# Optimization experiments

Measured on AMD Instinct MI355X. Metric: run time of the kernel, lower is better.

## Reference

```python
import jax, jax.numpy as jnp
import numpy as np
import math

L_MAX = 2; NRAD = 8; R_CUT = 3.5; N_LAYERS = 4; MUL0 = 32; MUL1 = 16
N_NODES = 20000; N_EDGES = 640000

# Orthonormal (Frobenius) basis of symmetric traceless 3x3 matrices for l=2
# component order: xy, yz, z^2, xz, x^2-y^2
_s2 = 1.0 / math.sqrt(2.0); _s6 = 1.0 / math.sqrt(6.0)
_B = np.zeros((5, 3, 3), dtype=np.float32)
_B[0, 0, 1] = _B[0, 1, 0] = _s2
_B[1, 1, 2] = _B[1, 2, 1] = _s2
_B[2, 0, 0] = _B[2, 1, 1] = -_s6; _B[2, 2, 2] = 2 * _s6
_B[3, 0, 2] = _B[3, 2, 0] = _s2
_B[4, 0, 0] = _s2; _B[4, 1, 1] = -_s2
B2 = jnp.asarray(_B)


def silu(x):
    return x * jax.nn.sigmoid(x)


def cutoff_fn(d):
    # CosineCutoff
    return 0.5 * (jnp.cos(d * math.pi / R_CUT) + 1.0) * (d < R_CUT).astype(d.dtype)


def smearing(d, means, betas):
    # ExpNormalSmearing with CosineCutoff envelope
    dc = jnp.clip(d, 1e-6, R_CUT)[:, None]          # [E,1]
    a = 5.0 / R_CUT
    b = jnp.clip(betas, 1e-6, None)
    return cutoff_fn(dc) * jnp.exp(-b * (jnp.exp(-a * dc) - means) ** 2)  # [E,NRAD]


def sph_harm(rh):
    # real spherical harmonics up to l=2, component normalization, (x,y,z) l=1 order
    y0 = jnp.ones_like(rh[:, :1])
    y1 = math.sqrt(3.0) * rh                                   # [E,3]
    rr = rh[:, :, None] * rh[:, None, :]                       # [E,3,3]
    tr = (rh * rh).sum(-1) / 3.0
    rr = rr - tr[:, None, None] * jnp.eye(3, dtype=rh.dtype)   # traceless
    y2 = math.sqrt(15.0) * jnp.einsum('eij,kij->ek', rr, B2)   # [E,5]
    return jnp.concatenate([y0, y1, y2], axis=-1)              # [E,9]


def _forward(pos, alpha, atom_emb, ne_emb, ne_dw, ne_db, ne_cw, ne_cb,
             means, betas, rad_w1, rad_b1, rad_w2, rad_b2,
             tp_w00, tp_w110, tp_w01, tp_w10, tp_w12,
             self_ws, self_wv, pre_ws, pre_wv, post_ws, post_wv,
             ln_g, ln_b, g_w1, g_b1, g_w2, g_b2, z, edge_index):
    N = pos.shape[0]
    src, dst = edge_index[0], edge_index[1]
    rvec = pos[dst] - pos[src]
    d = jnp.sqrt((rvec * rvec).sum(-1) + 1e-12)                # [E]
    rhat = rvec / d[:, None]

    rbf = smearing(d, means, betas)                            # [E,NRAD]
    # per-l radial coefficients (3 small MLPs, stacked on leading dim)
    h = silu(jnp.einsum('en,lnh->leh', rbf, rad_w1) + rad_b1[:, None, :])
    coeff = jnp.einsum('leh,lho->leo', h, rad_w2) + rad_b2[:, None, :]  # [3,E,1]

    Y = sph_harm(rhat)                                         # [E,9]
    eattr = jnp.concatenate([Y[:, :1] * coeff[0],
                             Y[:, 1:4] * coeff[1],
                             Y[:, 4:9] * coeff[2]], axis=-1)
    eattr = jnp.nan_to_num(eattr, nan=0.0, posinf=0.0, neginf=0.0)

    # AtomEncoder + NeighborEmbedding
    s = atom_emb[z]                                            # [N,32]
    C = cutoff_fn(d)
    W = (rbf @ ne_dw + ne_db) * C[:, None]                     # [E,32]
    xn = ne_emb[z]
    aggr = jax.ops.segment_sum(xn[dst] * W, src, num_segments=N)
    s = jnp.concatenate([s, aggr], axis=-1) @ ne_cw + ne_cb    # [N,32]
    v = jnp.zeros((N, MUL1, 3), dtype=s.dtype)                 # l=1 features

    e0, e1, e2 = eattr[:, :1], eattr[:, 1:4], eattr[:, 4:9]
    Qe = jnp.einsum('ek,kij->eij', e2, B2)                     # l=2 as sym traceless matrix

    for li in range(N_LAYERS):
        ss, vs = s[src], v[src]
        # CG tensor product paths (FullyConnectedTensorProduct node x edge -> node)
        m_s = (ss * e0) @ tp_w00[li] + jnp.einsum('evc,ec->ev', vs, e1) @ tp_w110[li]
        m_v = (jnp.einsum('ei,io->eo', ss, tp_w01[li])[:, :, None] * e1[:, None, :]
               + jnp.einsum('evc,vo->eoc', vs * e0[:, :, None], tp_w10[li])
               + jnp.einsum('evc,vo->eoc', jnp.einsum('eij,evj->evi', Qe, vs), tp_w12[li]))
        # alpha-weighted scatter-add aggregation
        ms = jax.ops.segment_sum(m_s * alpha, dst, num_segments=N)
        mv = jax.ops.segment_sum(m_v * alpha[:, :, None], dst, num_segments=N)
        # self interaction (o3.Linear, block-diag per l)
        s = s @ self_ws[li] + ms
        v = jnp.einsum('nvc,vo->noc', v, self_wv[li]) + mv
        # pre-linear -> gate -> post-linear
        ps = s @ pre_ws[li]                                    # [N,48] scalars+gates
        pv = jnp.einsum('nvc,vo->noc', v, pre_wv[li])
        sc = silu(ps[:, :MUL0])
        g = jax.nn.sigmoid(ps[:, MUL0:])
        v = pv * g[:, :, None]
        s = sc @ post_ws[li]
        v = jnp.einsum('nvc,vo->noc', v, post_wv[li])
        # layernorm on scalar channels
        mu = s.mean(-1, keepdims=True)
        var = ((s - mu) ** 2).mean(-1, keepdims=True)
        s = (s - mu) / jnp.sqrt(var + 1e-5) * ln_g[li] + ln_b[li]
        # geom2s: vector norms -> scalar residual
        vn = jnp.sqrt((v * v).sum(-1) + 1e-12)                 # [N,16]
        delta = silu(vn @ g_w1[li] + g_b1[li]) @ g_w2[li] + g_b2[li]
        s = s + delta
    return jnp.concatenate([s, v.reshape(N, MUL1 * 3)], axis=-1)  # [N,80]


def setup_inputs() -> dict:
    key = jax.random.key(0)
    ks = jax.random.split(key, 40)
    f32 = jnp.float32

    def rn(k, shape, fan):
        return jax.random.normal(k, shape, dtype=f32) / math.sqrt(fan)

    start = math.exp(-R_CUT)
    inp = {
        'pos': jax.random.uniform(ks[0], (N_NODES, 3), dtype=f32) * 10.0,
        'alpha': jax.random.uniform(ks[1], (N_EDGES, 1), dtype=f32),
        'atom_emb': rn(ks[2], (100, MUL0), 1.0),
        'ne_emb': rn(ks[3], (100, MUL0), 1.0),
        'ne_dw': rn(ks[4], (NRAD, MUL0), NRAD), 'ne_db': jnp.zeros((MUL0,), f32),
        'ne_cw': rn(ks[5], (2 * MUL0, MUL0), 2 * MUL0), 'ne_cb': jnp.zeros((MUL0,), f32),
        'means': jnp.linspace(start, 1.0, NRAD, dtype=f32),
        'betas': jnp.full((NRAD,), (2.0 / NRAD * (1.0 - start)) ** (-2), dtype=f32),
        'rad_w1': rn(ks[6], (3, NRAD, 256), NRAD), 'rad_b1': jnp.zeros((3, 256), f32),
        'rad_w2': rn(ks[7], (3, 256, 1), 256), 'rad_b2': jnp.zeros((3, 1), f32),
        'tp_w00': rn(ks[8], (N_LAYERS, MUL0, MUL0), MUL0),
        'tp_w110': rn(ks[9], (N_LAYERS, MUL1, MUL0), MUL1),
        'tp_w01': rn(ks[10], (N_LAYERS, MUL0, MUL1), MUL0),
        'tp_w10': rn(ks[11], (N_LAYERS, MUL1, MUL1), MUL1),
        'tp_w12': rn(ks[12], (N_LAYERS, MUL1, MUL1), MUL1),
        'self_ws': rn(ks[13], (N_LAYERS, MUL0, MUL0), MUL0),
        'self_wv': rn(ks[14], (N_LAYERS, MUL1, MUL1), MUL1),
        'pre_ws': rn(ks[15], (N_LAYERS, MUL0, MUL0 + MUL1), MUL0),
        'pre_wv': rn(ks[16], (N_LAYERS, MUL1, MUL1), MUL1),
        'post_ws': rn(ks[17], (N_LAYERS, MUL0, MUL0), MUL0),
        'post_wv': rn(ks[18], (N_LAYERS, MUL1, MUL1), MUL1),
        'ln_g': jnp.ones((N_LAYERS, MUL0), f32), 'ln_b': jnp.zeros((N_LAYERS, MUL0), f32),
        'g_w1': rn(ks[19], (N_LAYERS, MUL1, MUL1), MUL1), 'g_b1': jnp.zeros((N_LAYERS, MUL1), f32),
        'g_w2': rn(ks[20], (N_LAYERS, MUL1, MUL0), MUL1), 'g_b2': jnp.zeros((N_LAYERS, MUL0), f32),
        'z': jax.random.randint(ks[21], (N_NODES,), 0, 100, dtype=jnp.int32),
        'edge_index': jax.random.randint(ks[22], (2, N_EDGES), 0, N_NODES, dtype=jnp.int32),
    }
    return inp


def reference(pos, alpha, atom_emb, ne_emb, ne_dw, ne_db, ne_cw, ne_cb,
              means, betas, rad_w1, rad_b1, rad_w2, rad_b2,
              tp_w00, tp_w110, tp_w01, tp_w10, tp_w12,
              self_ws, self_wv, pre_ws, pre_wv, post_ws, post_wv,
              ln_g, ln_b, g_w1, g_b1, g_w2, g_b2, z, edge_index):
    return _forward(pos, alpha, atom_emb, ne_emb, ne_dw, ne_db, ne_cw, ne_cb,
                    means, betas, rad_w1, rad_b1, rad_w2, rad_b2,
                    tp_w00, tp_w110, tp_w01, tp_w10, tp_w12,
                    self_ws, self_wv, pre_ws, pre_wv, post_ws, post_wv,
                    ln_g, ln_b, g_w1, g_b1, g_w2, g_b2, z, edge_index)
```

## Files before the change

### kernel.cpp

```cpp
#include <hip/hip_runtime.h>

#define RCUT 3.5f
#define TTAB 2048

static __device__ __forceinline__ float sigmoidf_(float x) { return 1.0f / (1.0f + expf(-x)); }
static __device__ __forceinline__ float siluf(float x) { return x / (1.0f + expf(-x)); }
static __device__ __forceinline__ float san(float x) {
    return ((__float_as_uint(x) & 0x7F800000u) != 0x7F800000u) ? x : 0.f;
}

__global__ __launch_bounds__(256) void k_table(const float* means, const float* betas,
                        const float* rad_w1, const float* rad_b1,
                        const float* rad_w2, const float* rad_b2,
                        const float* ne_dw, const float* ne_db,
                        float* tab) {
    __shared__ float red[3][4];
    int i = blockIdx.x;
    int h = threadIdx.x;
    int lane = h & 63, wv = h >> 6;
    float d  = (float)i * (RCUT / (float)(TTAB - 1));
    float dc = fmaxf(d, 1e-6f);
    float C  = (dc < RCUT) ? 0.5f * (cosf(dc * (3.14159265358979f / RCUT)) + 1.0f) : 0.0f;
    float ex = expf(-(5.0f / RCUT) * dc);
    float rbf[8];
#pragma unroll
    for (int nn = 0; nn < 8; ++nn) {
        float b = fmaxf(betas[nn], 1e-6f);
        float t = ex - means[nn];
        rbf[nn] = C * expf(-b * t * t);
    }
    float con[3];
#pragma unroll
    for (int l = 0; l < 3; ++l) {
        float cc = rad_b1[l * 256 + h];
#pragma unroll
        for (int nn = 0; nn < 8; ++nn) cc += rbf[nn] * rad_w1[(l * 8 + nn) * 256 + h];
        con[l] = siluf(cc) * rad_w2[l * 256 + h];
    }
#pragma unroll
    for (int m = 1; m < 64; m <<= 1) {
        con[0] += __shfl_xor(con[0], m, 64);
        con[1] += __shfl_xor(con[1], m, 64);
        con[2] += __shfl_xor(con[2], m, 64);
    }
    if (lane == 0) { red[0][wv] = con[0]; red[1][wv] = con[1]; red[2][wv] = con[2]; }
    __syncthreads();
    if (h < 3)
        tab[i * 40 + h] = rad_b2[h] + red[h][0] + red[h][1] + red[h][2] + red[h][3];
    else if (h == 3)
        tab[i * 40 + 3] = 0.f;
    else if (h < 36) {
        int c = h - 4;
        float wvv = ne_db[c];
#pragma unroll
        for (int nn = 0; nn < 8; ++nn) wvv += rbf[nn] * ne_dw[nn * 32 + c];
        tab[i * 40 + h] = wvv * C;
    } else if (h < 40)
        tab[i * 40 + h] = 0.f;
}

__global__ void k_count(const int* ei, int* cnt_dst, int* cnt_src, int E) {
    int e = blockIdx.x * blockDim.x + threadIdx.x;
    if (e >= E) return;
    atomicAdd(cnt_dst + ei[E + e], 1);
    atomicAdd(cnt_src + ei[e], 1);
}

__global__ __launch_bounds__(1024) void k_scan2(const int* cntA, int* rowA, int* curA,
                        const int* cntB, int* rowB, int* curB, int n) {
    __shared__ int wsum[16];
    const int* cnt = blockIdx.x ? cntB : cntA;
    int* rowptr    = blockIdx.x ? rowB : rowA;
    int* cursor    = blockIdx.x ? curB : curA;
    int tid = threadIdx.x, lane = tid & 63, wv = tid >> 6;
    int per = (n + 1023) >> 10;
    int beg = tid * per; if (beg > n) beg = n;
    int end = beg + per; if (end > n) end = n;
    int s = 0;
    for (int i = beg; i < end; ++i) s += cnt[i];
    int v = s;
#pragma unroll
    for (int m = 1; m < 64; m <<= 1) {
        int t = __shfl_up(v, m, 64);
        if (lane >= m) v += t;
    }
    if (lane == 63) wsum[wv] = v;
    __syncthreads();
    int wbase = 0;
    for (int j = 0; j < wv; ++j) wbase += wsum[j];
    int run = wbase + v - s;
    for (int i = beg; i < end; ++i) {
        int val = cnt[i];
        rowptr[i] = run; cursor[i] = run;
        run += val;
    }
    if (tid == 1023) rowptr[n] = run;
}

__global__ void k_edge_fill(const float* pos, const float* alpha,
                            const int* ei, const float* tab, const int* z,
                            int* cur_dst, int* cur_src,
                            float4* rec, int2* rec_src, int E) {
    int e = blockIdx.x * blockDim.x + threadIdx.x;
    if (e >= E) return;
    int sn = ei[e], dn = ei[E + e];
    float rx = pos[dn * 3]     - pos[sn * 3];
    float ry = pos[dn * 3 + 1] - pos[sn * 3 + 1];
    float rz = pos[dn * 3 + 2] - pos[sn * 3 + 2];
    float d = sqrtf(rx * rx + ry * ry + rz * rz + 1e-12f);
    float inv = 1.0f / d;
    rx *= inv; ry *= inv; rz *= inv;
    float u = fminf(d, RCUT) * ((float)(TTAB - 1) / RCUT);
    int i0 = (int)u; if (i0 > TTAB - 2) i0 = TTAB - 2;
    float f = u - (float)i0;
    const float* t0 = tab + i0 * 40;
    float c0 = t0[0] + f * (t0[40] - t0[0]);
    float c1 = t0[1] + f * (t0[41] - t0[1]);
    float c2 = t0[2] + f * (t0[42] - t0[2]);
    float al = alpha[e];
    float ae0 = san(al * c0);
    float k1 = 1.73205081f * al * c1;
    float k2 = al * c2;
    float e20 = san(5.47722558f * rx * ry * k2);
    float e21 = san(5.47722558f * ry * rz * k2);
    float e22 = san(1.58113883f * (2.f * rz * rz - rx * rx - ry * ry) * k2);
    float e23 = san(5.47722558f * rx * rz * k2);
    float e24 = san(2.73861279f * (rx * rx - ry * ry) * k2);
    const float S2 = 0.70710678f, S6 = 0.40824829f;
    float q00 = -S6 * e22 + S2 * e24;
    float q01 = S2 * e20;
    float q02 = S2 * e23;
    float q11 = -S6 * e22 - S2 * e24;
    float q12 = S2 * e21;
    float q22 = 2.f * S6 * e22;
    int p = atomicAdd(cur_dst + dn, 1);
    size_t pb = (size_t)p * 4;
    rec[pb]     = make_float4(ae0, san(k1 * rx), san(k1 * ry), san(k1 * rz));
    rec[pb + 1] = make_float4(q00, q01, q02, q11);
    rec[pb + 2] = make_float4(q12, q22, __int_as_float(sn), 0.f);
    int p2 = atomicAdd(cur_src + sn, 1);
    float uc = fminf(u, (float)(TTAB - 1) - 1e-3f);
    rec_src[p2] = make_int2(__float_as_int(uc), z[dn]);
}

__global__ __launch_bounds__(256) void k_aggr(const int* row_src, const int2* recs,
        const int* z, const float* tab, const float* ne_emb, const float* atom_emb,
        const float* ne_cw, const float* ne_cb,
        float* sbuf, float* vbuf, int N) {
    __shared__ float part[4][64];
    __shared__ float cat[4][64];
    int wv = threadIdx.x >> 6, lane = threadIdx.x & 63;
    int n = blockIdx.x * 4 + wv;
    bool act = n < N;
    int g = lane >> 5, li = lane & 31;
    float acc = 0.f;
    if (act) {
        int r0 = row_src[n], r1 = row_src[n + 1];
        int half = (r1 - r0) >> 1;
        int kb = g ? (r0 + half) : r0;
        int ke = g ? r1 : (r0 + half);
        int k = kb;
        for (; k + 2 <= ke; k += 2) {
            int2 rA = recs[k], rB = recs[k + 1];
            float uA = __int_as_float(rA.x), uB = __int_as_float(rB.x);
            int iA = (int)uA, iB = (int)uB;
            float fA = uA - (float)iA, fB = uB - (float)iB;
            float wA0 = tab[iA * 40 + 4 + li], wA1 = tab[iA * 40 + 44 + li];
            float wB0 = tab[iB * 40 + 4 + li], wB1 = tab[iB * 40 + 44 + li];
            float eA = ne_emb[rA.y * 32 + li], eB = ne_emb[rB.y * 32 + li];
            acc += (wA0 + fA * (wA1 - wA0)) * eA + (wB0 + fB * (wB1 - wB0)) * eB;
        }
        for (; k < ke; ++k) {
            int2 r = recs[k];
            float u = __int_as_float(r.x);
            int i0 = (int)u; float f = u - (float)i0;
            float w0 = tab[i0 * 40 + 4 + li], w1 = tab[i0 * 40 + 44 + li];
            acc += (w0 + f * (w1 - w0)) * ne_emb[r.y * 32 + li];
        }
    }
    part[wv][lane] = acc;
    __builtin_amdgcn_wave_barrier();
    if (act && lane < 32) {
        cat[wv][lane] = atom_emb[z[n] * 32 + lane];
        cat[wv][32 + lane] = part[wv][lane] + part[wv][32 + lane];
    }
    __builtin_amdgcn_wave_barrier();
    if (act && lane < 32) {
        float so = ne_cb[lane];
        for (int j = 0; j < 64; ++j) so += cat[wv][j] * ne_cw[j * 32 + lane];
        sbuf[n * 32 + lane] = so;
    }
    if (act && lane < 48) vbuf[n * 48 + lane] = 0.f;
}

#define SBLK2(BIDX, X0, X1)                                                             \
    {                                                                                   \
        int e_ = ((BIDX) << 2) + 2 * h;                                                 \
        float4 A0 = eA[e_], A1 = eA[e_ + 1];                                            \
        a0  += X0 * A0.x + X1 * A1.x;                                                   \
        a1x += X0 * A0.y + X1 * A1.y;                                                   \
        a1y += X0 * A0.z + X1 * A1.z;                                                   \
        a1z += X0 * A0.w + X1 * A1.w;                                                   \
    }

#define VBLK1(BIDX, U, V, W)                                                            \
    {                                                                                   \
        int e_ = ((BIDX) << 2) + g;                                                     \
        float4 Aa = eA[e_];                                                             \
        float4 Qa = eQ[e_];                                                             \
        float2 Ra = eR[e_];                                                             \
        adv += U * Aa.y + V * Aa.z + W * Aa.w;                                          \
        a2x += U * Aa.x; a2y += V * Aa.x; a2z += W * Aa.x;                              \
        a3x += Qa.x * U + Qa.y * V + Qa.z * W;                                          \
        a3y += Qa.y * U + Qa.w * V + Ra.x * W;                                          \
        a3z += Qa.z * U + Ra.x * V + Ra.y * W;                                          \
    }

__global__ __launch_bounds__(128) void k_layer(const int* __restrict__ row_dst,
        const float4* __restrict__ rec,
        const float* __restrict__ sOld, const float* __restrict__ vOld,
        const float* w00, const float* w110, const float* w01,
        const float* w10, const float* w12,
        const float* self_ws, const float* self_wv,
        const float* pre_ws, const float* pre_wv,
        const float* post_ws, const float* post_wv,
        const float* ln_g, const float* ln_b,
        const float* g_w1, const float* g_b1,
        const float* g_w2, const float* g_b2,
        float* __restrict__ sNew, float* __restrict__ vNew,
        float* __restrict__ out, int N) {
    __shared__ __align__(16) float4 eA[64];
    __shared__ __align__(16) float4 eQ[64];
    __shared__ __align__(16) float2 eR[64];
    __shared__ __align__(16) int    eC[64];
    __shared__ float M[240];
    __shared__ float S[32], Vt[48], P[48];
    int wv = threadIdx.x >> 6, lane = threadIdx.x & 63;
    int n = blockIdx.x;
    int r0 = row_dst[n], r1 = row_dst[n + 1];
    int deg = r1 - r0;
    int cap = deg < 64 ? deg : 64;
    int nblk = cap >> 2;

    if (wv == 0) {
        if (lane < cap) {
            size_t idx = (size_t)(r0 + lane) * 4;
            float4 a  = rec[idx];
            float4 r2 = rec[idx + 2];
            eA[lane] = a;
            eR[lane] = make_float2(r2.x, r2.y);
            eC[lane] = __float_as_int(r2.z);
        }
        if (lane < 32) S[lane] = sOld[(size_t)n * 32 + lane];
    } else {
        if (lane < cap) {
            size_t idx = (size_t)(r0 + lane) * 4;
            eQ[lane] = rec[idx + 1];
        }
        if (lane < 48) Vt[(lane & 15) * 0 + (lane >> 4) * 16 + 0] = 0.f;
        if (lane < 48) Vt[(lane >> 4) * 16 + 0] = Vt[(lane >> 4) * 16 + 0];
        if (lane < 48) {
            int c_ = lane >> 4, o_ = lane & 15;
            Vt[c_ * 16 + o_] = vOld[(size_t)n * 48 + o_ * 3 + c_];
        }
    }
    __syncthreads();

    const int4* eC4 = (const int4*)eC;
    if (wv == 0) {
        int h = lane >> 5, d = lane & 31;
        float a0 = 0.f, a1x = 0.f, a1y = 0.f, a1z = 0.f;
        float xA0 = 0.f, xA1 = 0.f, xB0 = 0.f, xB1 = 0.f;
        if (nblk > 0) {
            int4 c4 = eC4[0];
            xA0 = sOld[(h ? c4.z : c4.x) * 32 + d];
            xA1 = sOld[(h ? c4.w : c4.y) * 32 + d];
        }
        if (nblk > 1) {
            int4 c4 = eC4[1];
            xB0 = sOld[(h ? c4.z : c4.x) * 32 + d];
            xB1 = sOld[(h ? c4.w : c4.y) * 32 + d];
        }
        int b = 0;
        for (; b + 2 <= nblk; b += 2) {
            int4 c40 = (b + 2 < nblk) ? eC4[b + 2] : make_int4(0, 0, 0, 0);
            int4 c41 = (b + 3 < nblk) ? eC4[b + 3] : make_int4(0, 0, 0, 0);
            float t0 = sOld[(h ? c40.z : c40.x) * 32 + d];
            float t1 = sOld[(h ? c40.w : c40.y) * 32 + d];
            float u0 = sOld[(h ? c41.z : c41.x) * 32 + d];
            float u1 = sOld[(h ? c41.w : c41.y) * 32 + d];
            SBLK2(b, xA0, xA1);
            SBLK2(b + 1, xB0, xB1);
            xA0 = t0; xA1 = t1; xB0 = u0; xB1 = u1;
        }
        if (b < nblk) { SBLK2(b, xA0, xA1); }
        for (int k = r0 + (nblk << 2); k < r1; ++k) {
            if (h == 0) {
                size_t kb = (size_t)k * 4;
                float4 A = rec[kb];
                int cc = __float_as_int(rec[kb + 2].z);
                float xx = sOld[cc * 32 + d];
                a0 += xx * A.x; a1x += xx * A.y; a1y += xx * A.z; a1z += xx * A.w;
            }
        }
        a0  += __shfl_xor(a0, 32, 64);
        a1x += __shfl_xor(a1x, 32, 64);
        a1y += __shfl_xor(a1y, 32, 64);
        a1z += __shfl_xor(a1z, 32, 64);
        if (lane < 32) {
            M[lane] = a0; M[32 + lane] = a1x; M[64 + lane] = a1y; M[96 + lane] = a1z;
        }
    } else {
        int g = lane >> 4, m = lane & 15;
        float adv = 0.f, a2x = 0.f, a2y = 0.f, a2z = 0.f, a3x = 0.f, a3y = 0.f, a3z = 0.f;
        float uA = 0.f, vA = 0.f, wA = 0.f, uB = 0.f, vB = 0.f, wB = 0.f;
        if (nblk > 0) {
            const float* vp = vOld + (size_t)eC[g] * 48 + m * 3;
            uA = vp[0]; vA = vp[1]; wA = vp[2];
        }
        if (nblk > 1) {
            const float* vp = vOld + (size_t)eC[4 + g] * 48 + m * 3;
            uB = vp[0]; vB = vp[1]; wB = vp[2];
        }
        int b = 0;
        for (; b + 2 <= nblk; b += 2) {
            int cn0 = (b + 2 < nblk) ? eC[(b + 2) * 4 + g] : 0;
            int cn1 = (b + 3 < nblk) ? eC[(b + 3) * 4 + g] : 0;
            const float* q0 = vOld + (size_t)cn0 * 48 + m * 3;
            const float* q1 = vOld + (size_t)cn1 * 48 + m * 3;
            float tu = q0[0], tv = q0[1], tw = q0[2];
            float su = q1[0], sv = q1[1], sw = q1[2];
            VBLK1(b, uA, vA, wA);
            VBLK1(b + 1, uB, vB, wB);
            uA = tu; vA = tv; wA = tw; uB = su; vB = sv; wB = sw;
        }
        if (b < nblk) { VBLK1(b, uA, vA, wA); }
        for (int k = r0 + (nblk << 2); k < r1; ++k) {
            if (g == 0) {
                size_t kb = (size_t)k * 4;
                float4 A = rec[kb];
                float4 Q = rec[kb + 1];
                float4 R2 = rec[kb + 2];
                int cc = __float_as_int(R2.z);
                const float* vp = vOld + (size_t)cc * 48 + m * 3;
                float vx = vp[0], vy = vp[1], vz = vp[2];
                adv += vx * A.y + vy * A.z + vz * A.w;
                a2x += vx * A.x; a2y += vy * A.x; a2z += vz * A.x;
                a3x += Q.x * vx + Q.y * vy + Q.z * vz;
                a3y += Q.y * vx + Q.w * vy + R2.x * vz;
                a3z += Q.z * vx + R2.x * vy + R2.y * vz;
            }
        }
        adv += __shfl_xor(adv, 16, 64); adv += __shfl_xor(adv, 32, 64);
        a2x += __shfl_xor(a2x, 16, 64); a2x += __shfl_xor(a2x, 32, 64);
        a2y += __shfl_xor(a2y, 16, 64); a2y += __shfl_xor(a2y, 32, 64);
        a2z += __shfl_xor(a2z, 16, 64); a2z += __shfl_xor(a2z, 32, 64);
        a3x += __shfl_xor(a3x, 16, 64); a3x += __shfl_xor(a3x, 32, 64);
        a3y += __shfl_xor(a3y, 16, 64); a3y += __shfl_xor(a3y, 32, 64);
        a3z += __shfl_xor(a3z, 16, 64); a3z += __shfl_xor(a3z, 32, 64);
        if (lane < 16) {
            M[128 + m] = adv;
            M[144 + m] = a2x; M[160 + m] = a2y; M[176 + m] = a2z;
            M[192 + m] = a3x; M[208 + m] = a3y; M[224 + m] = a3z;
        }
    }
    __syncthreads();

    float sln = 0.f, pv = 0.f;
    int c = lane >> 4, o = lane & 15;
    if (wv == 0) {
        float s1 = 0.f;
        if (lane < 32) {
            for (int i = 0; i < 32; ++i) s1 += M[i] * w00[i * 32 + lane];
            for (int v = 0; v < 16; ++v) s1 += M[128 + v] * w110[v * 32 + lane];
            for (int i = 0; i < 32; ++i) s1 += S[i] * self_ws[i * 32 + lane];
        }
        __builtin_amdgcn_wave_barrier();
        if (lane < 32) S[lane] = s1;
        __builtin_amdgcn_wave_barrier();
        float ps = 0.f;
        if (lane < 48) {
            for (int i = 0; i < 32; ++i) ps += S[i] * pre_ws[i * 48 + lane];
            P[lane] = ps;
        }
        __builtin_amdgcn_wave_barrier();
        float sc = (lane < 32) ? siluf(ps) : 0.f;
        if (lane < 32) S[lane] = sc;
        __builtin_amdgcn_wave_barrier();
        float s2 = 0.f;
        if (lane < 32) { for (int i = 0; i < 32; ++i) s2 += S[i] * post_ws[i * 32 + lane]; }
        float mu = s2;
        mu += __shfl_xor(mu, 1, 32); mu += __shfl_xor(mu, 2, 32);
        mu += __shfl_xor(mu, 4, 32); mu += __shfl_xor(mu, 8, 32); mu += __shfl_xor(mu, 16, 32);
        mu *= (1.0f / 32.0f);
        float t = s2 - mu;
        float var = t * t;
        var += __shfl_xor(var, 1, 32); var += __shfl_xor(var, 2, 32);
        var += __shfl_xor(var, 4, 32); var += __shfl_xor(var, 8, 32); var += __shfl_xor(var, 16, 32);
        var *= (1.0f / 32.0f);
        if (lane < 32) sln = t * rsqrtf(var + 1e-5f) * ln_g[lane] + ln_b[lane];
    } else {
        float v1 = 0.f;
        if (lane < 48) {
            for (int i = 0; i < 32; ++i) v1 += M[32 + c * 32 + i] * w01[i * 16 + o];
            for (int v = 0; v < 16; ++v) v1 += M[144 + c * 16 + v] * w10[v * 16 + o];
            for (int v = 0; v < 16; ++v) v1 += M[192 + c * 16 + v] * w12[v * 16 + o];
            for (int v = 0; v < 16; ++v) v1 += Vt[c * 16 + v] * self_wv[v * 16 + o];
        }
        __builtin_amdgcn_wave_barrier();
        if (lane < 48) Vt[lane] = v1;
        __builtin_amdgcn_wave_barrier();
        if (lane < 48) {
            for (int v = 0; v < 16; ++v) pv += Vt[c * 16 + v] * pre_wv[v * 16 + o];
        }
    }
    __syncthreads();

    float v3 = 0.f;
    if (wv == 1) {
        float v2 = (lane < 48) ? pv * sigmoidf_(P[32 + o]) : 0.f;
        __builtin_amdgcn_wave_barrier();
        if (lane < 48) Vt[lane] = v2;
        __builtin_amdgcn_wave_barrier();
        if (lane < 48) { for (int v = 0; v < 16; ++v) v3 += Vt[c * 16 + v] * post_wv[v * 16 + o]; }
        __builtin_amdgcn_wave_barrier();
        if (lane < 48) Vt[lane] = v3;
        __builtin_amdgcn_wave_barrier();
        if (lane < 16) {
            float vx = Vt[lane], vy = Vt[16 + lane], vz = Vt[32 + lane];
            P[lane] = sqrtf(vx * vx + vy * vy + vz * vz + 1e-12f);
        }
        __builtin_amdgcn_wave_barrier();
        if (lane < 16) {
            float x = g_b1[lane];
            for (int mm = 0; mm < 16; ++mm) x += P[mm] * g_w1[mm * 16 + lane];
            P[16 + lane] = siluf(x);
        }
    }
    __syncthreads();

    if (wv == 0) {
        if (lane < 32) {
            float dl = g_b2[lane];
            for (int oo = 0; oo < 16; ++oo) dl += P[16 + oo] * g_w2[oo * 32 + lane];
            float sfin = sln + dl;
            if (out) out[(size_t)n * 80 + lane] = sfin;
            else     sNew[(size_t)n * 32 + lane] = sfin;
        }
    } else {
        if (lane < 48) {
            if (out) out[(size_t)n * 80 + 32 + o * 3 + c] = v3;
            else     vNew[(size_t)n * 48 + o * 3 + c] = v3;
        }
    }
}

extern "C" void kernel_launch(void* const* d_in, const int* in_sizes, int n_in,
                              void* d_out, int out_size, void* d_ws, size_t ws_size,
                              hipStream_t stream) {
    auto F = [&](int i) { return (const float*)d_in[i]; };
    const int* z  = (const int*)d_in[31];
    const int* ei = (const int*)d_in[32];
    int N = in_sizes[0] / 3;
    int E = in_sizes[1];

    char* w = (char*)d_ws;
    size_t off = 0;
    auto take = [&](size_t bytes) { size_t cur = off; off += (bytes + 255) & ~(size_t)255; return cur; };
    float4* rec    = (float4*)(w + take((size_t)E * 64));
    int2*  rec_src = (int2*)(w + take((size_t)E * 8));
    float* tab     = (float*)(w + take((size_t)TTAB * 40 * 4));
    int* cnt_dst   = (int*)(w + take((size_t)2 * N * 4));
    int* cnt_src   = cnt_dst + N;
    int* row_dst   = (int*)(w + take((size_t)(N + 1) * 4));
    int* row_src   = (int*)(w + take((size_t)(N + 1) * 4));
    int* cur_dst   = (int*)(w + take((size_t)N * 4));
    int* cur_src   = (int*)(w + take((size_t)N * 4));
    float* sA      = (float*)(w + take((size_t)N * 32 * 4));
    float* vA      = (float*)(w + take((size_t)N * 48 * 4));
    float* sB      = (float*)(w + take((size_t)N * 32 * 4));
    float* vB      = (float*)(w + take((size_t)N * 48 * 4));

    hipMemsetAsync(cnt_dst, 0, (size_t)2 * N * 4, stream);

    k_table<<<TTAB, 256, 0, stream>>>(F(8), F(9), F(10), F(11),
                                      F(12), F(13), F(4), F(5), tab);
    k_count<<<(E + 255) / 256, 256, 0, stream>>>(ei, cnt_dst, cnt_src, E);
    k_scan2<<<2, 1024, 0, stream>>>(cnt_dst, row_dst, cur_dst,
                                    cnt_src, row_src, cur_src, N);
    k_edge_fill<<<(E + 255) / 256, 256, 0, stream>>>(F(0), F(1), ei, tab, z,
                                                     cur_dst, cur_src,
                                                     rec, rec_src, E);

    int nb = (N + 3) / 4;
    k_aggr<<<nb, 256, 0, stream>>>(row_src, rec_src, z, tab, F(3), F(2),
                                   F(6), F(7), sA, vA, N);

    float* sIn = sA; float* vIn = vA;
    float* sOut = sB; float* vOut = vB;
    for (int li = 0; li < 4; ++li) {
        float* outp = (li == 3) ? (float*)d_out : nullptr;
        k_layer<<<N, 128, 0, stream>>>(row_dst, rec,
                                        sIn, vIn,
                                        F(14) + li * 32 * 32, F(15) + li * 16 * 32,
                                        F(16) + li * 32 * 16, F(17) + li * 16 * 16,
                                        F(18) + li * 16 * 16,
                                        F(19) + li * 32 * 32, F(20) + li * 16 * 16,
                                        F(21) + li * 32 * 48, F(22) + li * 16 * 16,
                                        F(23) + li * 32 * 32, F(24) + li * 16 * 16,
                                        F(25) + li * 32, F(26) + li * 32,
                                        F(27) + li * 16 * 16, F(28) + li * 16,
                                        F(29) + li * 16 * 32, F(30) + li * 32,
                                        sOut, vOut, outp, N);
        float* ts = sIn; sIn = sOut; sOut = ts;
        float* tv = vIn; vIn = vOut; vOut = tv;
    }
}
```

Before: 572.3 us.

## Fold tensor-product, self and pre-linear weights into one precomputed matrix per layer

Result: slower. 703.3 us (+22.9%).

```diff
diff --git a/kernel.cpp b/kernel.cpp
--- a/kernel.cpp
+++ b/kernel.cpp
@@ -57,6 +57,62 @@
         tab[i * 40 + h] = wvv * C;
     } else if (h < 40)
         tab[i * 40 + h] = 0.f;
+}
+
+__global__ __launch_bounds__(256) void k_prep(
+        const float* w00, const float* w110, const float* w01, const float* w10,
+        const float* w12, const float* self_ws, const float* self_wv,
+        const float* pre_ws, const float* pre_wv,
+        const float* post_ws, const float* post_wv,
+        const float* g_w1, const float* g_w2, float* T) {
+    int li = blockIdx.x;
+    const float* W00  = w00  + li * 1024;
+    const float* W110 = w110 + li * 512;
+    const float* W01  = w01  + li * 512;
+    const float* W10  = w10  + li * 256;
+    const float* W12  = w12  + li * 256;
+    const float* SWS  = self_ws + li * 1024;
+    const float* SWV  = self_wv + li * 256;
+    const float* PRE  = pre_ws + li * 1536;
+    const float* PREV = pre_wv + li * 256;
+    const float* POST = post_ws + li * 1024;
+    const float* POSTV= post_wv + li * 256;
+    const float* G1   = g_w1 + li * 256;
+    const float* G2   = g_w2 + li * 512;
+    float* TL = T + (size_t)li * 7168;
+    for (int idx = threadIdx.x; idx < 3840; idx += 256) {
+        int o = idx / 80, k = idx % 80;
+        float acc = 0.f;
+        if (k < 32)      { for (int j = 0; j < 32; ++j) acc += W00[k * 32 + j] * PRE[j * 48 + o]; }
+        else if (k < 48) { for (int j = 0; j < 32; ++j) acc += W110[(k - 32) * 32 + j] * PRE[j * 48 + o]; }
+        else             { for (int j = 0; j < 32; ++j) acc += SWS[(k - 48) * 32 + j] * PRE[j * 48 + o]; }
+        TL[idx] = acc;
+    }
+    for (int idx = threadIdx.x; idx < 1280; idx += 256) {
+        int o = idx / 80, k = idx % 80;
+        float acc = 0.f;
+        if (k < 32)      { for (int j = 0; j < 16; ++j) acc += W01[k * 16 + j] * PREV[j * 16 + o]; }
+        else if (k < 48) { for (int j = 0; j < 16; ++j) acc += W10[(k - 32) * 16 + j] * PREV[j * 16 + o]; }
+        else if (k < 64) { for (int j = 0; j < 16; ++j) acc += W12[(k - 48) * 16 + j] * PREV[j * 16 + o]; }
+        else             { for (int j = 0; j < 16; ++j) acc += SWV[(k - 64) * 16 + j] * PREV[j * 16 + o]; }
+        TL[3840 + idx] = acc;
+    }
+    for (int idx = threadIdx.x; idx < 1024; idx += 256) {
+        int o = idx / 32, k = idx % 32;
+        TL[5120 + idx] = POST[k * 32 + o];
+    }
+    for (int idx = threadIdx.x; idx < 256; idx += 256) {
+        int o = idx / 16, k = idx % 16;
+        TL[6144 + idx] = POSTV[k * 16 + o];
+    }
+    for (int idx = threadIdx.x; idx < 256; idx += 256) {
+        int o = idx / 16, k = idx % 16;
+        TL[6400 + idx] = G1[k * 16 + o];
+    }
+    for (int idx = threadIdx.x; idx < 512; idx += 256) {
+        int o = idx / 16, k = idx % 16;
+        TL[6656 + idx] = G2[k * 32 + o];
+    }
 }
 
 __global__ void k_count(const int* ei, int* cnt_dst, int* cnt_src, int E) {
@@ -216,31 +272,33 @@
         a3z += Qa.z * U + Ra.x * V + Ra.y * W;                                          \
     }
 
+#define DOT4(ACC, W4, X4) { float4 w_ = (W4), x_ = (X4);                                \
+    ACC += w_.x * x_.x + w_.y * x_.y + w_.z * x_.z + w_.w * x_.w; }
+
 __global__ __launch_bounds__(128) void k_layer(const int* __restrict__ row_dst,
         const float4* __restrict__ rec,
         const float* __restrict__ sOld, const float* __restrict__ vOld,
-        const float* w00, const float* w110, const float* w01,
-        const float* w10, const float* w12,
-        const float* self_ws, const float* self_wv,
-        const float* pre_ws, const float* pre_wv,
-        const float* post_ws, const float* post_wv,
-        const float* ln_g, const float* ln_b,
-        const float* g_w1, const float* g_b1,
-        const float* g_w2, const float* g_b2,
+        const float* __restrict__ T,
+        const float* __restrict__ ln_g, const float* __restrict__ ln_b,
+        const float* __restrict__ g_b1, const float* __restrict__ g_b2,
         float* __restrict__ sNew, float* __restrict__ vNew,
         float* __restrict__ out, int N) {
     __shared__ __align__(16) float4 eA[64];
     __shared__ __align__(16) float4 eQ[64];
     __shared__ __align__(16) float2 eR[64];
     __shared__ __align__(16) int    eC[64];
-    __shared__ float M[240];
-    __shared__ float S[32], Vt[48], P[48];
+    __shared__ __align__(16) float XS[80];
+    __shared__ __align__(16) float XV[3][80];
+    __shared__ __align__(16) float SC[32];
+    __shared__ __align__(16) float V2[48];
+    __shared__ __align__(16) float P[48];
     int wv = threadIdx.x >> 6, lane = threadIdx.x & 63;
     int n = blockIdx.x;
     int r0 = row_dst[n], r1 = row_dst[n + 1];
     int deg = r1 - r0;
     int cap = deg < 64 ? deg : 64;
     int nblk = cap >> 2;
+    int c = lane >> 4, o = lane & 15;
 
     if (wv == 0) {
         if (lane < cap) {
@@ -251,18 +309,13 @@
             eR[lane] = make_float2(r2.x, r2.y);
             eC[lane] = __float_as_int(r2.z);
         }
-        if (lane < 32) S[lane] = sOld[(size_t)n * 32 + lane];
+        if (lane < 32) XS[48 + lane] = sOld[(size_t)n * 32 + lane];
     } else {
         if (lane < cap) {
             size_t idx = (size_t)(r0 + lane) * 4;
             eQ[lane] = rec[idx + 1];
         }
-        if (lane < 48) Vt[(lane & 15) * 0 + (lane >> 4) * 16 + 0] = 0.f;
-        if (lane < 48) Vt[(lane >> 4) * 16 + 0] = Vt[(lane >> 4) * 16 + 0];
-        if (lane < 48) {
-            int c_ = lane >> 4, o_ = lane & 15;
-            Vt[c_ * 16 + o_] = vOld[(size_t)n * 48 + o_ * 3 + c_];
-        }
+        if (lane < 48) XV[c][64 + o] = vOld[(size_t)n * 48 + o * 3 + c];
     }
     __syncthreads();
 
@@ -308,7 +361,8 @@
         a1y += __shfl_xor(a1y, 32, 64);
         a1z += __shfl_xor(a1z, 32, 64);
         if (lane < 32) {
-            M[lane] = a0; M[32 + lane] = a1x; M[64 + lane] = a1y; M[96 + lane] = a1z;
+            XS[lane] = a0;
+            XV[0][lane] = a1x; XV[1][lane] = a1y; XV[2][lane] = a1z;
         }
     } else {
         int g = lane >> 4, m = lane & 15;
@@ -359,36 +413,51 @@
         a3y += __shfl_xor(a3y, 16, 64); a3y += __shfl_xor(a3y, 32, 64);
         a3z += __shfl_xor(a3z, 16, 64); a3z += __shfl_xor(a3z, 32, 64);
         if (lane < 16) {
-            M[128 + m] = adv;
-            M[144 + m] = a2x; M[160 + m] = a2y; M[176 + m] = a2z;
-            M[192 + m] = a3x; M[208 + m] = a3y; M[224 + m] = a3z;
+            XS[32 + m] = adv;
+            XV[0][32 + m] = a2x; XV[1][32 + m] = a2y; XV[2][32 + m] = a2z;
+            XV[0][48 + m] = a3x; XV[1][48 + m] = a3y; XV[2][48 + m] = a3z;
         }
     }
     __syncthreads();
 
-    float sln = 0.f, pv = 0.f;
-    int c = lane >> 4, o = lane & 15;
+    const float* TA  = T;
+    const float* TV  = T + 3840;
+    const float* TP  = T + 5120;
+    const float* TPV = T + 6144;
+    const float* TG1 = T + 6400;
+    const float* TG2 = T + 6656;
+
+    float ps = 0.f, pv = 0.f;
     if (wv == 0) {
-        float s1 = 0.f;
-        if (lane < 32) {
-            for (int i = 0; i < 32; ++i) s1 += M[i] * w00[i * 32 + lane];
-            for (int v = 0; v < 16; ++v) s1 += M[128 + v] * w110[v * 32 + lane];
-            for (int i = 0; i < 32; ++i) s1 += S[i] * self_ws[i * 32 + lane];
-        }
-        __builtin_amdgcn_wave_barrier();
-        if (lane < 32) S[lane] = s1;
-        __builtin_amdgcn_wave_barrier();
-        float ps = 0.f;
         if (lane < 48) {
-            for (int i = 0; i < 32; ++i) ps += S[i] * pre_ws[i * 48 + lane];
-            P[lane] = ps;
-        }
-        __builtin_amdgcn_wave_barrier();
+            const float4* Tr = (const float4*)(TA + lane * 80);
+            const float4* X4 = (const float4*)XS;
+#pragma unroll
+            for (int k = 0; k < 20; ++k) DOT4(ps, Tr[k], X4[k]);
+            if (lane >= 32) P[lane] = ps;
+        }
+    } else {
+        if (lane < 48) {
+            const float4* Tr = (const float4*)(TV + o * 80);
+            const float4* X4 = (const float4*)(&XV[c][0]);
+#pragma unroll
+            for (int k = 0; k < 20; ++k) DOT4(pv, Tr[k], X4[k]);
+        }
+    }
+    __syncthreads();
+
+    float sln = 0.f, v3 = 0.f;
+    if (wv == 0) {
         float sc = (lane < 32) ? siluf(ps) : 0.f;
-        if (lane < 32) S[lane] = sc;
+        if (lane < 32) SC[lane] = sc;
         __builtin_amdgcn_wave_barrier();
         float s2 = 0.f;
-        if (lane < 32) { for (int i = 0; i < 32; ++i) s2 += S[i] * post_ws[i * 32 + lane]; }
+        if (lane < 32) {
+            const float4* Tr = (const float4*)(TP + lane * 32);
+            const float4* X4 = (const float4*)SC;
+#pragma unroll
+            for (int k = 0; k < 8; ++k) DOT4(s2, Tr[k], X4[k]);
+        }
         float mu = s2;
         mu += __shfl_xor(mu, 1, 32); mu += __shfl_xor(mu, 2, 32);
         mu += __shfl_xor(mu, 4, 32); mu += __shfl_xor(mu, 8, 32); mu += __shfl_xor(mu, 16, 32);
@@ -400,40 +469,29 @@
         var *= (1.0f / 32.0f);
         if (lane < 32) sln = t * rsqrtf(var + 1e-5f) * ln_g[lane] + ln_b[lane];
     } else {
-        float v1 = 0.f;
-        if (lane < 48) {
-            for (int i = 0; i < 32; ++i) v1 += M[32 + c * 32 + i] * w01[i * 16 + o];
-            for (int v = 0; v < 16; ++v) v1 += M[144 + c * 16 + v] * w10[v * 16 + o];
-            for (int v = 0; v < 16; ++v) v1 += M[192 + c * 16 + v] * w12[v * 16 + o];
-            for (int v = 0; v < 16; ++v) v1 += Vt[c * 16 + v] * self_wv[v * 16 + o];
-        }
-        __builtin_amdgcn_wave_barrier();
-        if (lane < 48) Vt[lane] = v1;
+        float v2 = (lane < 48) ? pv * sigmoidf_(P[32 + o]) : 0.f;
+        if (lane < 48) V2[c * 16 + o] = v2;
         __builtin_amdgcn_wave_barrier();
         if (lane < 48) {
-            for (int v = 0; v < 16; ++v) pv += Vt[c * 16 + v] * pre_wv[v * 16 + o];
-        }
-    }
-    __syncthreads();
-
-    float v3 = 0.f;
-    if (wv == 1) {
-        float v2 = (lane < 48) ? pv * sigmoidf_(P[32 + o]) : 0.f;
+            const float4* Tr = (const float4*)(TPV + o * 16);
+            const float4* X4 = (const float4*)(V2 + c * 16);
+#pragma unroll
+            for (int k = 0; k < 4; ++k) DOT4(v3, Tr[k], X4[k]);
+        }
         __builtin_amdgcn_wave_barrier();
-        if (lane < 48) Vt[lane] = v2;
-        __builtin_amdgcn_wave_barrier();
-        if (lane < 48) { for (int v = 0; v < 16; ++v) v3 += Vt[c * 16 + v] * post_wv[v * 16 + o]; }
-        __builtin_amdgcn_wave_barrier();
-        if (lane < 48) Vt[lane] = v3;
+        if (lane < 48) V2[c * 16 + o] = v3;
         __builtin_amdgcn_wave_barrier();
         if (lane < 16) {
-            float vx = Vt[lane], vy = Vt[16 + lane], vz = Vt[32 + lane];
+            float vx = V2[lane], vy = V2[16 + lane], vz = V2[32 + lane];
             P[lane] = sqrtf(vx * vx + vy * vy + vz * vz + 1e-12f);
         }
         __builtin_amdgcn_wave_barrier();
         if (lane < 16) {
+            const float4* Tr = (const float4*)(TG1 + lane * 16);
+            const float4* X4 = (const float4*)P;
             float x = g_b1[lane];
-            for (int mm = 0; mm < 16; ++mm) x += P[mm] * g_w1[mm * 16 + lane];
+#pragma unroll
+            for (int k = 0; k < 4; ++k) DOT4(x, Tr[k], X4[k]);
             P[16 + lane] = siluf(x);
         }
     }
@@ -441,8 +499,11 @@
 
     if (wv == 0) {
         if (lane < 32) {
+            const float4* Tr = (const float4*)(TG2 + lane * 16);
+            const float4* X4 = (const float4*)(P + 16);
             float dl = g_b2[lane];
-            for (int oo = 0; oo < 16; ++oo) dl += P[16 + oo] * g_w2[oo * 32 + lane];
+#pragma unroll
+            for (int k = 0; k < 4; ++k) DOT4(dl, Tr[k], X4[k]);
             float sfin = sln + dl;
             if (out) out[(size_t)n * 80 + lane] = sfin;
             else     sNew[(size_t)n * 32 + lane] = sfin;
@@ -470,6 +531,7 @@
     float4* rec    = (float4*)(w + take((size_t)E * 64));
     int2*  rec_src = (int2*)(w + take((size_t)E * 8));
     float* tab     = (float*)(w + take((size_t)TTAB * 40 * 4));
+    float* Tw      = (float*)(w + take((size_t)4 * 7168 * 4));
     int* cnt_dst   = (int*)(w + take((size_t)2 * N * 4));
     int* cnt_src   = cnt_dst + N;
     int* row_dst   = (int*)(w + take((size_t)(N + 1) * 4));
@@ -485,6 +547,9 @@
 
     k_table<<<TTAB, 256, 0, stream>>>(F(8), F(9), F(10), F(11),
                                       F(12), F(13), F(4), F(5), tab);
+    k_prep<<<4, 256, 0, stream>>>(F(14), F(15), F(16), F(17), F(18),
+                                  F(19), F(20), F(21), F(22), F(23), F(24),
+                                  F(27), F(29), Tw);
     k_count<<<(E + 255) / 256, 256, 0, stream>>>(ei, cnt_dst, cnt_src, E);
     k_scan2<<<2, 1024, 0, stream>>>(cnt_dst, row_dst, cur_dst,
                                     cnt_src, row_src, cur_src, N);
@@ -501,17 +566,11 @@
     for (int li = 0; li < 4; ++li) {
         float* outp = (li == 3) ? (float*)d_out : nullptr;
         k_layer<<<N, 128, 0, stream>>>(row_dst, rec,
-                                        sIn, vIn,
-                                        F(14) + li * 32 * 32, F(15) + li * 16 * 32,
-                                        F(16) + li * 32 * 16, F(17) + li * 16 * 16,
-                                        F(18) + li * 16 * 16,
-                                        F(19) + li * 32 * 32, F(20) + li * 16 * 16,
-                                        F(21) + li * 32 * 48, F(22) + li * 16 * 16,
-                                        F(23) + li * 32 * 32, F(24) + li * 16 * 16,
-                                        F(25) + li * 32, F(26) + li * 32,
-                                        F(27) + li * 16 * 16, F(28) + li * 16,
-                                        F(29) + li * 16 * 32, F(30) + li * 32,
-                                        sOut, vOut, outp, N);
+                                       sIn, vIn,
+                                       Tw + (size_t)li * 7168,
+                                       F(25) + li * 32, F(26) + li * 32,
+                                       F(28) + li * 16, F(30) + li * 32,
+                                       sOut, vOut, outp, N);
         float* ts = sIn; sIn = sOut; sOut = ts;
         float* tv = vIn; vIn = vOut; vOut = tv;
     }
```
